# Performance work log

Measured on AMD Instinct MI355X. Metric: run time of the kernel, lower is better.

## Reference

```python
import jax, jax.numpy as jnp
import numpy as np

N = 65536   # batch
G = 7       # grid
C = 2       # classes (cats vs dogs)
A = 3       # anchors


def _bce(p, t):
    return -(t * jnp.log(p) + (1.0 - t) * jnp.log(1.0 - p))


def _iou(a, b):
    # a, b: [..., 4] boxes in (cx, cy, w, h) format
    ax1, ay1 = a[..., 0] - a[..., 2] / 2, a[..., 1] - a[..., 3] / 2
    ax2, ay2 = a[..., 0] + a[..., 2] / 2, a[..., 1] + a[..., 3] / 2
    bx1, by1 = b[..., 0] - b[..., 2] / 2, b[..., 1] - b[..., 3] / 2
    bx2, by2 = b[..., 0] + b[..., 2] / 2, b[..., 1] + b[..., 3] / 2
    iw = jnp.clip(jnp.minimum(ax2, bx2) - jnp.maximum(ax1, bx1), 0.0)
    ih = jnp.clip(jnp.minimum(ay2, by2) - jnp.maximum(ay1, by1), 0.0)
    inter = iw * ih
    union = (ax2 - ax1) * (ay2 - ay1) + (bx2 - bx1) * (by2 - by1) - inter
    return inter / (union + 1e-9)


def setup_inputs():
    key = jax.random.key(0)
    k1, k2, k3, k4 = jax.random.split(key, 4)
    # probabilities / box params must lie strictly in (0,1) for BCE and log()
    bbox_ = jax.random.uniform(k1, (N, 15, G, G), dtype=jnp.float32, minval=0.01, maxval=0.99)
    bbox = jax.random.uniform(k2, (N, 5, G, G), dtype=jnp.float32, minval=0.01, maxval=0.99)
    cls_ = jax.random.normal(k3, (N, C), dtype=jnp.float32)
    cls = jax.random.randint(k4, (N,), 1, 3).astype(jnp.int64)  # labels in {1,2}
    return {"bbox_": bbox_, "cls_": cls_, "bbox": bbox, "cls": cls}


def reference(bbox_, cls_, bbox, cls):
    n = bbox.shape[0]
    bidx = jnp.arange(n)

    # classification: CrossEntropyLoss (mean) with labels cls-1
    logp = jax.nn.log_softmax(cls_, axis=-1)
    ce = -jnp.mean(jnp.take_along_axis(logp, (cls - 1)[:, None], axis=1))

    # argmax cell of GT objectness map per sample
    probs = bbox[:, 0]                       # [N,7,7]
    m = jnp.argmax(probs.reshape(n, -1), axis=1)
    i, j = m // G, m % G                     # [N], [N]

    cell_gt = bbox[bidx, :, i, j]            # [N,5]
    cell_pr = bbox_[bidx, :, i, j].reshape(n, A, 5)  # [N,3,5]

    jf = j.astype(bbox.dtype)
    if_ = i.astype(bbox.dtype)

    # target box in global coords
    tgt = jnp.stack([(cell_gt[:, 1] + jf) / G, (cell_gt[:, 2] + if_) / G,
                     cell_gt[:, 3], cell_gt[:, 4]], axis=-1)          # [N,4]
    # anchor boxes in global coords
    anc = jnp.stack([(cell_pr[:, :, 1] + jf[:, None]) / G,
                     (cell_pr[:, :, 2] + if_[:, None]) / G,
                     cell_pr[:, :, 3], cell_pr[:, :, 4]], axis=-1)    # [N,3,4]

    best = jnp.argmax(_iou(anc, tgt[:, None, :]), axis=1)             # [N]

    # target objectness maps: best anchor channel gets GT prob map
    target_prob = jnp.zeros((n, A, G, G), dtype=bbox.dtype)
    target_prob = target_prob.at[bidx, best].set(probs)

    # coordinate BCE (sum) + size L1-of-logs (sum) at the matched cell/anchor
    best_box = cell_pr[bidx, best]           # [N,5]
    coord = jnp.sum(_bce(best_box[:, 1:3], cell_gt[:, 1:3]))
    size = jnp.sum(jnp.abs(jnp.log(best_box[:, 3:5]) - jnp.log(cell_gt[:, 3:5])))

    # per-anchor objectness BCE (mean over N*49 each)
    prob_loss = (jnp.mean(_bce(bbox_[:, 0], target_prob[:, 0]))
                 + jnp.mean(_bce(bbox_[:, 5], target_prob[:, 1]))
                 + jnp.mean(_bce(bbox_[:, 10], target_prob[:, 2])))

    return ce + coord + size + prob_loss
```

## Files before the change

kernel.cpp:

```cpp
#include <hip/hip_runtime.h>
#include <math.h>


static constexpr int GG_ = 49;

__global__ void zero_kernel(float* out) { if (threadIdx.x == 0) out[0] = 0.0f; }

__global__ __launch_bounds__(256) void loss_kernel(
    const float* __restrict__ pr_all,
    const float* __restrict__ cls_logits,
    const float* __restrict__ gt_all,
    const int*   __restrict__ cls_lbl,
    float* __restrict__ out, int N)
{
    const int lane   = threadIdx.x & 63;
    const int wid    = blockIdx.x * (blockDim.x >> 6) + (threadIdx.x >> 6);
    const int nwaves = gridDim.x * (blockDim.x >> 6);
    const float invG   = 1.0f / 7.0f;
    const float invN   = 1.0f / (float)N;
    const float invN49 = 1.0f / ((float)N * 49.0f);

    float acc = 0.0f;

    for (int n = wid; n < N; n += nwaves) {
        const float* gt = gt_all + (size_t)n * (5  * GG_);
        const float* pr = pr_all + (size_t)n * (15 * GG_);

        float t = -1.0f;
        if (lane < GG_) t = gt[lane];

        float v = t; int idx = lane;
        #pragma unroll
        for (int off = 32; off; off >>= 1) {
            float v2 = __shfl_xor(v, off);
            int   i2 = __shfl_xor(idx, off);
            if (v2 > v || (v2 == v && i2 < idx)) { v = v2; idx = i2; }
        }
        const int m  = idx;
        const int mi = m / 7, mj = m - mi * 7;
        const float jf = (float)mj, if_ = (float)mi;

        float p0 = 0.5f, p1 = 0.5f, p2 = 0.5f;
        if (lane < GG_) {
            p0 = pr[lane];
            p1 = pr[5  * GG_ + lane];
            p2 = pr[10 * GG_ + lane];
        }

        float cellv = 0.0f;
        if (lane >= 1 && lane <= 4) {
            cellv = gt[lane * GG_ + m];
        } else if (lane >= 5 && lane < 17) {
            int k = lane - 5;
            int a = k >> 2, c = k & 3;
            cellv = pr[(5 * a + 1 + c) * GG_ + m];
        }

        const float g1 = __shfl(cellv, 1);
        const float g2 = __shfl(cellv, 2);
        const float g3 = __shfl(cellv, 3);
        const float g4 = __shfl(cellv, 4);

        const float tx  = (g1 + jf) * invG;
        const float ty  = (g2 + if_) * invG;
        const float tx1 = tx - g3 * 0.5f, tx2 = tx + g3 * 0.5f;
        const float ty1 = ty - g4 * 0.5f, ty2 = ty + g4 * 0.5f;
        const float tarea = (tx2 - tx1) * (ty2 - ty1);

        int best = 0; float bestIoU = -1.0f;
        #pragma unroll
        for (int a = 0; a < 3; a++) {
            float c1 = __shfl(cellv, 5 + 4 * a + 0);
            float c2 = __shfl(cellv, 5 + 4 * a + 1);
            float c3 = __shfl(cellv, 5 + 4 * a + 2);
            float c4 = __shfl(cellv, 5 + 4 * a + 3);
            float ax  = (c1 + jf) * invG;
            float ay  = (c2 + if_) * invG;
            float ax1 = ax - c3 * 0.5f, ax2 = ax + c3 * 0.5f;
            float ay1 = ay - c4 * 0.5f, ay2 = ay + c4 * 0.5f;
            float iw = fminf(ax2, tx2) - fmaxf(ax1, tx1); iw = fmaxf(iw, 0.0f);
            float ih = fminf(ay2, ty2) - fmaxf(ay1, ty1); ih = fmaxf(ih, 0.0f);
            float inter = iw * ih;
            float uni   = (ax2 - ax1) * (ay2 - ay1) + tarea - inter;
            float iou   = inter / (uni + 1e-9f);
            if (iou > bestIoU) { bestIoU = iou; best = a; }
        }

        const float px = __shfl(cellv, 5 + 4 * best + 0);
        const float py = __shfl(cellv, 5 + 4 * best + 1);
        const float pw = __shfl(cellv, 5 + 4 * best + 2);
        const float ph = __shfl(cellv, 5 + 4 * best + 3);

        float s = 0.0f;
        if (lane < GG_) {
            float l1p0 = __logf(1.0f - p0);
            float l1p1 = __logf(1.0f - p1);
            float l1p2 = __logf(1.0f - p2);
            s = -(l1p0 + l1p1 + l1p2);
            float pb   = (best == 0) ? p0 : ((best == 1) ? p1 : p2);
            float l1pb = (best == 0) ? l1p0 : ((best == 1) ? l1p1 : l1p2);
            s -= t * (__logf(pb) - l1pb);
        }
        acc += s * invN49;

        if (lane == 0) {
            float coord = -(g1 * __logf(px) + (1.0f - g1) * __logf(1.0f - px))
                          -(g2 * __logf(py) + (1.0f - g2) * __logf(1.0f - py));
            float size  = fabsf(__logf(pw) - __logf(g3))
                        + fabsf(__logf(ph) - __logf(g4));
            float x0 = cls_logits[2 * n], x1 = cls_logits[2 * n + 1];
            int   c  = cls_lbl[n] - 1;
            float mx  = fmaxf(x0, x1);
            float lse = mx + __logf(__expf(x0 - mx) + __expf(x1 - mx));
            float lp  = ((c == 0) ? x0 : x1) - lse;
            acc += coord + size - lp * invN;
        }
    }

    #pragma unroll
    for (int off = 32; off; off >>= 1) acc += __shfl_xor(acc, off);
    __shared__ float wsum[4];
    if (lane == 0) wsum[threadIdx.x >> 6] = acc;
    __syncthreads();
    if (threadIdx.x == 0) {
        atomicAdd(out, wsum[0] + wsum[1] + wsum[2] + wsum[3]);
    }
}

extern "C" void kernel_launch(void* const* d_in, const int* in_sizes, int n_in,
                              void* d_out, int out_size, void* d_ws, size_t ws_size,
                              hipStream_t stream) {
    const float* bbox_p = (const float*)d_in[0];
    const float* cls_p  = (const float*)d_in[1];
    const float* bbox_g = (const float*)d_in[2];
    const int*   cls_l  = (const int*)d_in[3];
    float* out = (float*)d_out;
    const int N = in_sizes[3];

    hipLaunchKernelGGL(zero_kernel, dim3(1), dim3(64), 0, stream, out);
    hipLaunchKernelGGL(loss_kernel, dim3(2048), dim3(256), 0, stream,
                       bbox_p, cls_p, bbox_g, cls_l, out, N);
}
```

Measured before the change: 309.8 us.

## Use one wave per sample, ballot argmax, and two-pass deterministic reduction

Replaces the grid-stride loop with one wave per sample across N/4 blocks. The argmax now uses a max shuffle plus a ballot/ffs instead of paired value-index shuffles, and all logs are issued right after the loads. The per-sample scalar terms are split across lanes 49-53 rather than done serially on lane 0. The atomic add into the output is replaced by per-block partials in workspace followed by a single-block reduce kernel, which adds a second launch and a serial reduce over 16K partials.

```diff
diff --git a/kernel.cpp b/kernel.cpp
--- a/kernel.cpp
+++ b/kernel.cpp
@@ -4,48 +4,52 @@
 
 static constexpr int GG_ = 49;
 
-__global__ void zero_kernel(float* out) { if (threadIdx.x == 0) out[0] = 0.0f; }
-
 __global__ __launch_bounds__(256) void loss_kernel(
     const float* __restrict__ pr_all,
     const float* __restrict__ cls_logits,
     const float* __restrict__ gt_all,
     const int*   __restrict__ cls_lbl,
-    float* __restrict__ out, int N)
+    float* __restrict__ partial, int N)
 {
-    const int lane   = threadIdx.x & 63;
-    const int wid    = blockIdx.x * (blockDim.x >> 6) + (threadIdx.x >> 6);
-    const int nwaves = gridDim.x * (blockDim.x >> 6);
+    const int lane = threadIdx.x & 63;
+    const int n    = blockIdx.x * 4 + (threadIdx.x >> 6);
     const float invG   = 1.0f / 7.0f;
     const float invN   = 1.0f / (float)N;
-    const float invN49 = 1.0f / ((float)N * 49.0f);
+    const float invN49 = invN * (1.0f / 49.0f);
 
     float acc = 0.0f;
 
-    for (int n = wid; n < N; n += nwaves) {
+    if (n < N) {
         const float* gt = gt_all + (size_t)n * (5  * GG_);
         const float* pr = pr_all + (size_t)n * (15 * GG_);
 
-        float t = -1.0f;
-        if (lane < GG_) t = gt[lane];
-
-        float v = t; int idx = lane;
-        #pragma unroll
-        for (int off = 32; off; off >>= 1) {
-            float v2 = __shfl_xor(v, off);
-            int   i2 = __shfl_xor(idx, off);
-            if (v2 > v || (v2 == v && i2 < idx)) { v = v2; idx = i2; }
-        }
-        const int m  = idx;
-        const int mi = m / 7, mj = m - mi * 7;
-        const float jf = (float)mj, if_ = (float)mi;
-
-        float p0 = 0.5f, p1 = 0.5f, p2 = 0.5f;
+        float t = -1.0f, p0 = 0.5f, p1 = 0.5f, p2 = 0.5f;
         if (lane < GG_) {
+            t  = gt[lane];
             p0 = pr[lane];
             p1 = pr[5  * GG_ + lane];
             p2 = pr[10 * GG_ + lane];
         }
+        float x0 = 0.0f, x1 = 0.0f; int cl = 0;
+        if (lane == 53) {
+            x0 = cls_logits[2 * n];
+            x1 = cls_logits[2 * n + 1];
+            cl = cls_lbl[n] - 1;
+        }
+
+        float lp0 = 0, lp1 = 0, lp2 = 0, l1p0 = 0, l1p1 = 0, l1p2 = 0;
+        if (lane < GG_) {
+            lp0  = __logf(p0);         lp1  = __logf(p1);         lp2  = __logf(p2);
+            l1p0 = __logf(1.0f - p0);  l1p1 = __logf(1.0f - p1);  l1p2 = __logf(1.0f - p2);
+        }
+
+        float v = t;
+        #pragma unroll
+        for (int off = 32; off; off >>= 1) v = fmaxf(v, __shfl_xor(v, off));
+        unsigned long long msk = __ballot(t == v);
+        const int m  = __ffsll(msk) - 1;
+        const int mi = m / 7, mj = m - mi * 7;
+        const float jf = (float)mj, if_ = (float)mi;
 
         float cellv = 0.0f;
         if (lane >= 1 && lane <= 4) {
@@ -91,29 +95,27 @@
         const float pw = __shfl(cellv, 5 + 4 * best + 2);
         const float ph = __shfl(cellv, 5 + 4 * best + 3);
 
-        float s = 0.0f;
         if (lane < GG_) {
-            float l1p0 = __logf(1.0f - p0);
-            float l1p1 = __logf(1.0f - p1);
-            float l1p2 = __logf(1.0f - p2);
-            s = -(l1p0 + l1p1 + l1p2);
-            float pb   = (best == 0) ? p0 : ((best == 1) ? p1 : p2);
+            float s = -(l1p0 + l1p1 + l1p2);
+            float lpb  = (best == 0) ? lp0  : ((best == 1) ? lp1  : lp2);
             float l1pb = (best == 0) ? l1p0 : ((best == 1) ? l1p1 : l1p2);
-            s -= t * (__logf(pb) - l1pb);
+            s -= t * (lpb - l1pb);
+            acc += s * invN49;
         }
-        acc += s * invN49;
 
-        if (lane == 0) {
-            float coord = -(g1 * __logf(px) + (1.0f - g1) * __logf(1.0f - px))
-                          -(g2 * __logf(py) + (1.0f - g2) * __logf(1.0f - py));
-            float size  = fabsf(__logf(pw) - __logf(g3))
-                        + fabsf(__logf(ph) - __logf(g4));
-            float x0 = cls_logits[2 * n], x1 = cls_logits[2 * n + 1];
-            int   c  = cls_lbl[n] - 1;
+        if (lane == 49) {
+            acc += -(g1 * __logf(px) + (1.0f - g1) * __logf(1.0f - px));
+        } else if (lane == 50) {
+            acc += -(g2 * __logf(py) + (1.0f - g2) * __logf(1.0f - py));
+        } else if (lane == 51) {
+            acc += fabsf(__logf(pw) - __logf(g3));
+        } else if (lane == 52) {
+            acc += fabsf(__logf(ph) - __logf(g4));
+        } else if (lane == 53) {
             float mx  = fmaxf(x0, x1);
             float lse = mx + __logf(__expf(x0 - mx) + __expf(x1 - mx));
-            float lp  = ((c == 0) ? x0 : x1) - lse;
-            acc += coord + size - lp * invN;
+            float lp  = ((cl == 0) ? x0 : x1) - lse;
+            acc += -lp * invN;
         }
     }
 
@@ -122,9 +124,22 @@
     __shared__ float wsum[4];
     if (lane == 0) wsum[threadIdx.x >> 6] = acc;
     __syncthreads();
-    if (threadIdx.x == 0) {
-        atomicAdd(out, wsum[0] + wsum[1] + wsum[2] + wsum[3]);
-    }
+    if (threadIdx.x == 0)
+        partial[blockIdx.x] = wsum[0] + wsum[1] + wsum[2] + wsum[3];
+}
+
+__global__ __launch_bounds__(256) void reduce_kernel(
+    const float* __restrict__ partial, float* __restrict__ out, int M)
+{
+    const int lane = threadIdx.x & 63;
+    float s = 0.0f;
+    for (int i = threadIdx.x; i < M; i += 256) s += partial[i];
+    #pragma unroll
+    for (int off = 32; off; off >>= 1) s += __shfl_xor(s, off);
+    __shared__ float wsum[4];
+    if (lane == 0) wsum[threadIdx.x >> 6] = s;
+    __syncthreads();
+    if (threadIdx.x == 0) out[0] = wsum[0] + wsum[1] + wsum[2] + wsum[3];
 }
 
 extern "C" void kernel_launch(void* const* d_in, const int* in_sizes, int n_in,
@@ -137,7 +152,11 @@
     float* out = (float*)d_out;
     const int N = in_sizes[3];
 
-    hipLaunchKernelGGL(zero_kernel, dim3(1), dim3(64), 0, stream, out);
-    hipLaunchKernelGGL(loss_kernel, dim3(2048), dim3(256), 0, stream,
-                       bbox_p, cls_p, bbox_g, cls_l, out, N);
+    const int nblocks = (N + 3) / 4;
+    float* partial = (float*)d_ws;
+
+    hipLaunchKernelGGL(loss_kernel, dim3(nblocks), dim3(256), 0, stream,
+                       bbox_p, cls_p, bbox_g, cls_l, partial, N);
+    hipLaunchKernelGGL(reduce_kernel, dim3(1), dim3(256), 0, stream,
+                       partial, out, nblocks);
 }
```

Measured after the change: 311.6 us. About the same (+0.6%).
